# Kernel tuning notes

Measured on AMD Instinct MI355X. Metric: run time of the kernel, lower is better.

## Reference

```python
import jax, jax.numpy as jnp
import numpy as np

N = 50000      # nodes
E = 800000     # edges (avg degree 16)
C = 128        # hidden_channels
L = 3          # CGConv layers actually executed (forward uses layers[1:] of 4)
K = 10         # category_number
BN_EPS = 1e-5


def setup_inputs() -> dict:
    key = jax.random.key(0)
    ks = jax.random.split(key, 18)
    s = 0.05
    inp = {
        "x": jax.random.normal(ks[0], (N, 7), dtype=jnp.float32),
        "edge_index": jax.random.randint(ks[1], (2, E), 0, N, dtype=jnp.int64),
        "edge_attr": jax.random.normal(ks[2], (E, 6), dtype=jnp.float32),
        # node / edge encoders
        "node_W": jax.random.normal(ks[3], (C, 7), dtype=jnp.float32) * s,
        "node_b": jax.random.normal(ks[4], (C,), dtype=jnp.float32) * s,
        "edge_W": jax.random.normal(ks[5], (C, 6), dtype=jnp.float32) * s,
        "edge_b": jax.random.normal(ks[6], (C,), dtype=jnp.float32) * s,
        # CGConv layers (stacked over L): lin_f, lin_s take concat(x_i, x_j, e) of dim 3C
        "Wf": jax.random.normal(ks[7], (L, C, 3 * C), dtype=jnp.float32) * s,
        "bf": jax.random.normal(ks[8], (L, C), dtype=jnp.float32) * s,
        "Ws": jax.random.normal(ks[9], (L, C, 3 * C), dtype=jnp.float32) * s,
        "bs": jax.random.normal(ks[10], (L, C), dtype=jnp.float32) * s,
        # batch norm (eval-mode: running stats)
        "gamma": jnp.ones((L, C), dtype=jnp.float32),
        "beta": jnp.zeros((L, C), dtype=jnp.float32),
        "bn_mean": jax.random.normal(ks[11], (L, C), dtype=jnp.float32) * s,
        "bn_var": jax.random.uniform(ks[12], (L, C), dtype=jnp.float32) + 0.5,
        # classifier head
        "lin_W": jax.random.normal(ks[13], (K, C), dtype=jnp.float32) * s,
        "lin_b": jax.random.normal(ks[14], (K,), dtype=jnp.float32) * s,
    }
    return inp


def _gcn_forward(x, edge_index, edge_attr, node_W, node_b, edge_W, edge_b,
                 Wf, bf, Ws, bs, gamma, beta, bn_mean, bn_var, lin_W, lin_b):
    h = x @ node_W.T + node_b                      # [N, C]
    e = edge_attr @ edge_W.T + edge_b              # [E, C]
    src = edge_index[0]                            # x_j (source)
    dst = edge_index[1]                            # x_i (target / aggregation index)
    n = h.shape[0]
    c = h.shape[1]
    for l in range(Wf.shape[0]):
        # split concat weight: z = [x_i | x_j | e]; W z = Wi x_i + Wj x_j + We e
        Wfi, Wfj, Wfe = Wf[l, :, :c], Wf[l, :, c:2 * c], Wf[l, :, 2 * c:]
        Wsi, Wsj, Wse = Ws[l, :, :c], Ws[l, :, c:2 * c], Ws[l, :, 2 * c:]
        # node-side projections once per node, then gather per edge
        hf_i, hf_j = h @ Wfi.T, h @ Wfj.T          # [N, C]
        hs_i, hs_j = h @ Wsi.T, h @ Wsj.T
        zf = hf_i[dst] + hf_j[src] + e @ Wfe.T + bf[l]   # [E, C]
        zs = hs_i[dst] + hs_j[src] + e @ Wse.T + bs[l]
        msg = jax.nn.sigmoid(zf) * jax.nn.softplus(zs)   # CGConv gated message
        agg = jax.ops.segment_max(msg, dst, num_segments=n)  # max aggregation
        agg = jnp.where(jnp.isneginf(agg), 0.0, agg)     # nodes with no in-edges -> 0
        # batch norm (eval) on aggregated messages
        agg = (agg - bn_mean[l]) * jax.lax.rsqrt(bn_var[l] + BN_EPS) * gamma[l] + beta[l]
        h = h + agg                                       # CGConv residual
    return h @ lin_W.T + lin_b, h


def reference(x, edge_index, edge_attr, node_W, node_b, edge_W, edge_b,
              Wf, bf, Ws, bs, gamma, beta, bn_mean, bn_var, lin_W, lin_b):
    return _gcn_forward(x, edge_index, edge_attr, node_W, node_b, edge_W, edge_b,
                        Wf, bf, Ws, bs, gamma, beta, bn_mean, bn_var, lin_W, lin_b)
```

## Files before the change

### kernel.cpp

```cpp
#include <hip/hip_runtime.h>

#define N_NODES 50000
#define N_EDGES 800000
#define C 128
#define NLAYERS 3
#define KOUT 10
#define BN_EPS 1e-5f
#define NGROUP_PAD 3128
#define SBLK 196
#define MAXDEG 64
#define LOG2E 1.4426950408889634f
#define LN2   0.6931471805599453f

#if __has_builtin(__builtin_amdgcn_exp2f)
#define EXP2(x) __builtin_amdgcn_exp2f(x)
#else
#define EXP2(x) exp2f(x)
#endif
#if __has_builtin(__builtin_amdgcn_logf)
#define LOG2(x) __builtin_amdgcn_logf(x)
#else
#define LOG2(x) log2f(x)
#endif
#if __has_builtin(__builtin_amdgcn_rcpf)
#define RCP(x) __builtin_amdgcn_rcpf(x)
#else
#define RCP(x) (1.f / (x))
#endif

typedef float v2f __attribute__((ext_vector_type(2)));
typedef __attribute__((ext_vector_type(4))) float f32x4;
typedef __attribute__((ext_vector_type(8))) short s16x8;

__device__ __forceinline__ float bf2f(unsigned short u) {
    return __uint_as_float(((unsigned int)u) << 16);
}
__device__ __forceinline__ unsigned short f2bf(float f) {
    unsigned int b = __float_as_uint(f);
    b += 0x7fff + ((b >> 16) & 1);
    return (unsigned short)(b >> 16);
}
__device__ __forceinline__ float blo(unsigned int u) { return __uint_as_float(u << 16); }
__device__ __forceinline__ float bhi(unsigned int u) { return __uint_as_float(u & 0xffff0000u); }
__device__ __forceinline__ unsigned int pk2bf(float lo, float hi) {
    return (unsigned int)f2bf(lo) | ((unsigned int)f2bf(hi) << 16);
}
__device__ __forceinline__ float loadf(const void* p, long long i, int bf) {
    return bf ? bf2f(((const unsigned short*)p)[i]) : ((const float*)p)[i];
}
__device__ __forceinline__ int loadi(const void* p, long long i, int i64) {
    return i64 ? (int)((const long long*)p)[i] : ((const int*)p)[i];
}

__device__ __forceinline__ int h16f_off(int n, int chunk) {
    int g = n >> 4, rr = n & 15;
    int ks = chunk >> 2, kq = chunk & 3;
    return (((g * 4 + ks) * 64) + kq * 16 + rr) * 8;
}
__device__ __forceinline__ int perm_o(int o) {
    int g = o >> 7, c = o & 127;
    return ((g & 2) ? 256 : 0) + ((c >> 2) << 3) + ((g & 1) ? 4 : 0) + (c & 3);
}

__global__ __launch_bounds__(256) void setup_kernel(
    int* __restrict__ cnt, const unsigned int* __restrict__ gbits,
    const unsigned int* __restrict__ ebits, int* __restrict__ flags) {
    int b = blockIdx.x, t = threadIdx.x;
    if (b < SBLK) {
        int i = b * 256 + t;
        if (i < N_NODES) cnt[i] = 0;
    } else {
        __shared__ int nz;
        if (t == 0) nz = 0;
        __syncthreads();
        if (t < 63 && ebits[t * 2 + 1] != 0u) atomicAdd(&nz, 1);
        __syncthreads();
        if (t == 0) {
            flags[0] = (gbits[0] == 0x3F803F80u) ? 1 : 0;
            flags[1] = (nz == 0) ? 1 : 0;
        }
    }
}

__global__ __launch_bounds__(256) void work1_kernel(
    const void* __restrict__ x, const void* __restrict__ node_W,
    const void* __restrict__ node_b, float* __restrict__ h,
    unsigned short* __restrict__ h16f,
    const void* __restrict__ Wf, const void* __restrict__ Ws,
    const void* __restrict__ bfv, const void* __restrict__ bsv,
    const void* __restrict__ edge_W, const void* __restrict__ edge_b,
    const void* __restrict__ gamma, const void* __restrict__ beta,
    const void* __restrict__ bn_mean, const void* __restrict__ bn_var,
    const void* __restrict__ lin_W, const void* __restrict__ lin_b,
    unsigned short* __restrict__ W2, float* __restrict__ Wfold,
    float* __restrict__ bfold,
    float* __restrict__ bnA, float* __restrict__ bnB,
    float* __restrict__ linWf, float* __restrict__ linbf,
    const int* __restrict__ flags) {
    int f = flags[0];
    int b = blockIdx.x, t = threadIdx.x;
    if (b < 6250) {
        int gtid = b * 256 + t;
        int n = gtid >> 5;
        if (n >= N_NODES) return;
        int q = gtid & 31, c0 = q * 4;
        float xv[7];
#pragma unroll
        for (int j = 0; j < 7; ++j) xv[j] = loadf(x, (long long)n * 7 + j, f);
        float4 acc;
        float* ap = (float*)&acc;
#pragma unroll
        for (int i = 0; i < 4; ++i) {
            int c = c0 + i;
            float a = loadf(node_b, c, f);
#pragma unroll
            for (int j = 0; j < 7; ++j)
                a = fmaf(xv[j], loadf(node_W, (long long)c * 7 + j, f), a);
            ap[i] = a;
        }
        ((float4*)h)[(long long)n * 32 + q] = acc;
        ushort4 s;
        s.x = f2bf(ap[0]); s.y = f2bf(ap[1]); s.z = f2bf(ap[2]); s.w = f2bf(ap[3]);
        *((ushort4*)(h16f + h16f_off(n, q >> 1) + (q & 1) * 4)) = s;
    } else {
        int bb = b - 6250;
        if (bb < 768) {
            int idx = bb * 256 + t;
            int k = idx & 127;
            int o = (idx >> 7) & 511;
            int l = idx >> 16;
            int c = o & 127;
            int g = o >> 7;
            long long base = (long long)l * C * 3 * C + (long long)c * 3 * C;
            float v;
            if (g == 0)      v = loadf(Wf, base + k, f);
            else if (g == 1) v = loadf(Ws, base + k, f);
            else if (g == 2) v = loadf(Wf, base + C + k, f);
            else             v = loadf(Ws, base + C + k, f);
            v *= LOG2E;
            int p = perm_o(o);
            int rt = p >> 4, rr = p & 15;
            int ch = k >> 3, j = k & 7;
            int ks = ch >> 2, kq = ch & 3;
            size_t w2i = ((((size_t)l * 32 + rt) * 4 + ks) * 64 + kq * 16 + rr) * 8 + j;
            W2[w2i] = f2bf(v);
        } else if (bb < 774) {
            if (t >= 128) return;
            int cc = bb - 768;
            int l = cc >> 1, s = cc & 1;
            const void* W = s ? Ws : Wf;
            const void* bias = s ? bsv : bfv;
            long long wbase = (long long)l * C * 3 * C + (long long)t * 3 * C + 2 * C;
            float acc[6] = {0.f, 0.f, 0.f, 0.f, 0.f, 0.f};
            float bacc = 0.f;
            for (int k = 0; k < C; ++k) {
                float w = loadf(W, wbase + k, f);
#pragma unroll
                for (int j = 0; j < 6; ++j)
                    acc[j] = fmaf(w, loadf(edge_W, k * 6 + j, f), acc[j]);
                bacc = fmaf(w, loadf(edge_b, k, f), bacc);
            }
#pragma unroll
            for (int j = 0; j < 6; ++j) Wfold[cc * 768 + j * C + t] = acc[j] * LOG2E;
            bfold[cc * C + t] = (bacc + loadf(bias, l * C + t, f)) * LOG2E;
        } else if (bb < 779) {
            int idx = (bb - 774) * 256 + t;
            if (idx < KOUT * C) linWf[idx] = loadf(lin_W, idx, f);
            if (idx < KOUT) linbf[idx] = loadf(lin_b, idx, f);
        } else {
            int idx = (bb - 779) * 256 + t;
            if (idx < NLAYERS * C) {
                float mn = loadf(bn_mean, idx, f);
                float vr = loadf(bn_var, idx, f);
                float gm = loadf(gamma, idx, f);
                float bt = loadf(beta, idx, f);
                float a = gm * rsqrtf(vr + BN_EPS);
                bnA[idx] = a * LN2;
                bnB[idx] = bt - mn * a;
            }
        }
    }
}

__global__ __launch_bounds__(256) void scatter_kernel(
    const void* __restrict__ edge_index, const void* __restrict__ edge_attr,
    int* __restrict__ cnt, float* __restrict__ eatt,
    const int* __restrict__ flags) {
    int f = flags[0], i64 = flags[1];
    int e = blockIdx.x * blockDim.x + threadIdx.x;
    if (e >= N_EDGES) return;
    int src = loadi(edge_index, e, i64);
    int dst = loadi(edge_index, (long long)N_EDGES + e, i64);
    int pos = atomicAdd(&cnt[dst], 1);
    if (pos >= MAXDEG) return;
    uint4 E;
    if (f) {
        const unsigned short* ea = (const unsigned short*)edge_attr;
        unsigned int b0 = ea[e * 6 + 0], b1 = ea[e * 6 + 1], b2 = ea[e * 6 + 2];
        unsigned int b3 = ea[e * 6 + 3], b4 = ea[e * 6 + 4], b5 = ea[e * 6 + 5];
        E.x = b0 | (b1 << 16); E.y = b2 | (b3 << 16); E.z = b4 | (b5 << 16);
    } else {
        const float* ea = (const float*)edge_attr;
        E.x = pk2bf(ea[e * 6 + 0], ea[e * 6 + 1]);
        E.y = pk2bf(ea[e * 6 + 2], ea[e * 6 + 3]);
        E.z = pk2bf(ea[e * 6 + 4], ea[e * 6 + 5]);
    }
    E.w = (unsigned int)src;
    ((uint4*)eatt)[(size_t)dst * MAXDEG + pos] = E;
}

__global__ __launch_bounds__(256) void gemm_kernel(
    const unsigned short* __restrict__ h16f,
    const unsigned short* __restrict__ W2,
    unsigned short* __restrict__ hcat) {
    __shared__ float smem[4 * 16 * 66];
    float* ls = smem;
    int wid = threadIdx.x >> 6, lane = threadIdx.x & 63;
    int mtile = blockIdx.x >> 1;
    int n0 = (blockIdx.x & 1) * 256 + wid * 64;
    int m0 = mtile * 64, g0 = mtile * 4;
    int rt0 = n0 >> 4;
    int cw = lane & 15, kq = lane >> 4, rw = kq * 4;
    const s16x8* Ap = (const s16x8*)h16f;
    const s16x8* Bp = (const s16x8*)W2;
    f32x4 acc[4][4];
#pragma unroll
    for (int i = 0; i < 4; ++i)
#pragma unroll
        for (int j = 0; j < 4; ++j) acc[i][j] = (f32x4){0.f, 0.f, 0.f, 0.f};
#pragma unroll
    for (int ks = 0; ks < 4; ++ks) {
        s16x8 a[4], b[4];
#pragma unroll
        for (int mt = 0; mt < 4; ++mt)
            a[mt] = Ap[((g0 + mt) * 4 + ks) * 64 + lane];
#pragma unroll
        for (int nt = 0; nt < 4; ++nt)
            b[nt] = Bp[((rt0 + nt) * 4 + ks) * 64 + lane];
#pragma unroll
        for (int mt = 0; mt < 4; ++mt)
#pragma unroll
            for (int nt = 0; nt < 4; ++nt)
                acc[mt][nt] = __builtin_amdgcn_mfma_f32_16x16x32_bf16(
                    a[mt], b[nt], acc[mt][nt], 0, 0, 0);
    }
    float* lw = ls + wid * (16 * 66);
    int er = lane >> 2, ecg = lane & 3;
#pragma unroll
    for (int mt = 0; mt < 4; ++mt) {
#pragma unroll
        for (int nt = 0; nt < 4; ++nt)
#pragma unroll
            for (int reg = 0; reg < 4; ++reg)
                lw[(rw + reg) * 66 + nt * 16 + cw] = acc[mt][nt][reg];
        int m = m0 + mt * 16 + er;
        float vv[16];
#pragma unroll
        for (int t2 = 0; t2 < 8; ++t2) {
            float2 w = *((float2*)&lw[er * 66 + ecg * 16 + t2 * 2]);
            vv[t2 * 2] = w.x; vv[t2 * 2 + 1] = w.y;
        }
        if (m < N_NODES) {
            ushort4 u0, u1, u2, u3;
            u0.x=f2bf(vv[0]);  u0.y=f2bf(vv[1]);  u0.z=f2bf(vv[2]);  u0.w=f2bf(vv[3]);
            u1.x=f2bf(vv[4]);  u1.y=f2bf(vv[5]);  u1.z=f2bf(vv[6]);  u1.w=f2bf(vv[7]);
            u2.x=f2bf(vv[8]);  u2.y=f2bf(vv[9]);  u2.z=f2bf(vv[10]); u2.w=f2bf(vv[11]);
            u3.x=f2bf(vv[12]); u3.y=f2bf(vv[13]); u3.z=f2bf(vv[14]); u3.w=f2bf(vv[15]);
            ushort4* dst = (ushort4*)(hcat + (size_t)m * 512 + n0 + ecg * 16);
            dst[0] = u0; dst[1] = u1; dst[2] = u2; dst[3] = u3;
        }
    }
}

__global__ __launch_bounds__(64) void agg_kernel(
    const float* __restrict__ eatt,
    const int* __restrict__ cnt, const unsigned short* __restrict__ hcat,
    const float* __restrict__ Wfold, const float* __restrict__ bfold,
    float* __restrict__ h, unsigned short* __restrict__ h16f,
    const float* __restrict__ bnA, const float* __restrict__ bnB,
    void* __restrict__ outp,
    int layer, const int* __restrict__ flags) {
    int f = flags[0];
    int n = blockIdx.x;
    int lane = threadIdx.x & 63;
    int half = lane >> 5;
    int q = lane & 31;
    int c0 = q * 4;

    float4 bA = *((const float4*)(bnA + layer * C + c0));
    float4 bB = *((const float4*)(bnB + layer * C + c0));
    int d = cnt[n];
    if (d > MAXDEG) d = MAXDEG;
    float mf[4] = {0.f, 0.f, 0.f, 0.f};

    const float* wfp = Wfold + (2 * layer + 0) * 768;
    const float* wsp = Wfold + (2 * layer + 1) * 768;
    v2f wf2[6][2], ws2[6][2];
#pragma unroll
    for (int j = 0; j < 6; ++j) {
        float4 a = *((const float4*)(wfp + j * C + c0));
        float4 b = *((const float4*)(wsp + j * C + c0));
        wf2[j][0] = (v2f){a.x, a.y}; wf2[j][1] = (v2f){a.z, a.w};
        ws2[j][0] = (v2f){b.x, b.y}; ws2[j][1] = (v2f){b.z, b.w};
    }
    float4 bfv = *((const float4*)(bfold + (2 * layer + 0) * C + c0));
    float4 bsv = *((const float4*)(bfold + (2 * layer + 1) * C + c0));
    uint4 ib = ((const uint4*)hcat)[(long long)n * 64 + q];
    v2f bf0 = (v2f){blo(ib.x) + bfv.x, bhi(ib.x) + bfv.y};
    v2f bf1 = (v2f){blo(ib.y) + bfv.z, bhi(ib.y) + bfv.w};
    v2f bs0 = (v2f){blo(ib.z) + bsv.x, bhi(ib.z) + bsv.y};
    v2f bs1 = (v2f){blo(ib.w) + bsv.z, bhi(ib.w) + bsv.w};

    auto body = [&](v2f hf0, v2f hf1, v2f hs0, v2f hs1, const float* ea) {
        v2f vf0 = bf0 + hf0, vf1 = bf1 + hf1;
        v2f vs0 = bs0 + hs0, vs1 = bs1 + hs1;
#pragma unroll
        for (int j = 0; j < 6; ++j) {
            v2f ej = (v2f){ea[j], ea[j]};
            vf0 = __builtin_elementwise_fma(ej, wf2[j][0], vf0);
            vf1 = __builtin_elementwise_fma(ej, wf2[j][1], vf1);
            vs0 = __builtin_elementwise_fma(ej, ws2[j][0], vs0);
            vs1 = __builtin_elementwise_fma(ej, ws2[j][1], vs1);
        }
        float zf[4] = {vf0.x, vf0.y, vf1.x, vf1.y};
        float zs[4] = {vs0.x, vs0.y, vs1.x, vs1.y};
#pragma unroll
        for (int i = 0; i < 4; ++i) {
            float sg = RCP(1.f + EXP2(-zf[i]));
            float sp = fmaxf(zs[i], 0.f) + LOG2(1.f + EXP2(-fabsf(zs[i])));
            mf[i] = fmaxf(mf[i], sg * sp);
        }
    };

    const uint4* hb = (const uint4*)hcat;
    const uint4* ep = (const uint4*)eatt + (size_t)n * MAXDEG;
    for (int p = half; p < d; p += 2) {
        uint4 E = ep[p];
        uint4 jb = hb[(long long)E.w * 64 + 32 + q];
        float ea[6] = {blo(E.x), bhi(E.x), blo(E.y), bhi(E.y), blo(E.z), bhi(E.z)};
        body((v2f){blo(jb.x), bhi(jb.x)}, (v2f){blo(jb.y), bhi(jb.y)},
             (v2f){blo(jb.z), bhi(jb.z)}, (v2f){blo(jb.w), bhi(jb.w)}, ea);
    }
#pragma unroll
    for (int i = 0; i < 4; ++i) mf[i] = fmaxf(mf[i], __shfl_xor(mf[i], 32));

    if (half == 0) {
        float4 hv = ((float4*)h)[(long long)n * 32 + q];
        float* hp = (float*)&hv;
        const float* bAp = (const float*)&bA;
        const float* bBp = (const float*)&bB;
#pragma unroll
        for (int i = 0; i < 4; ++i)
            hp[i] += mf[i] * bAp[i] + bBp[i];
        ((float4*)h)[(long long)n * 32 + q] = hv;
        {
            ushort4 s;
            s.x = f2bf(hp[0]); s.y = f2bf(hp[1]); s.z = f2bf(hp[2]); s.w = f2bf(hp[3]);
            *((ushort4*)(h16f + h16f_off(n, q >> 1) + (q & 1) * 4)) = s;
        }
        if (layer == NLAYERS - 1) {
            if (f) {
                ushort4 s;
                s.x = f2bf(hp[0]); s.y = f2bf(hp[1]); s.z = f2bf(hp[2]); s.w = f2bf(hp[3]);
                *((ushort4*)((unsigned short*)outp + N_NODES * KOUT + n * C + c0)) = s;
            } else {
                *((float4*)((float*)outp + N_NODES * KOUT + n * C + c0)) = hv;
            }
        }
    }
}

__global__ __launch_bounds__(256) void out_kernel(
    const float* __restrict__ h, const float* __restrict__ linWf,
    const float* __restrict__ linbf, void* __restrict__ out,
    const int* __restrict__ flags) {
    int f = flags[0];
    int g = blockIdx.x * 16 + (threadIdx.x >> 4);
    int l16 = threadIdx.x & 15;
    if (g >= N_NODES) return;
    const float4* hr = (const float4*)(h + (long long)g * C) + l16 * 2;
    float4 a0 = hr[0], a1 = hr[1];
    float res = 0.f;
#pragma unroll
    for (int k = 0; k < KOUT; ++k) {
        const float4* wr = (const float4*)(linWf + (long long)k * C) + l16 * 2;
        float4 w0 = wr[0], w1 = wr[1];
        float p = a0.x * w0.x + a0.y * w0.y + a0.z * w0.z + a0.w * w0.w
                + a1.x * w1.x + a1.y * w1.y + a1.z * w1.z + a1.w * w1.w;
        p += __shfl_xor(p, 1); p += __shfl_xor(p, 2);
        p += __shfl_xor(p, 4); p += __shfl_xor(p, 8);
        if (l16 == k) res = p + linbf[k];
    }
    if (l16 < KOUT) {
        long long idx = (long long)g * KOUT + l16;
        if (f) ((unsigned short*)out)[idx] = f2bf(res);
        else   ((float*)out)[idx] = res;
    }
}

extern "C" void kernel_launch(void* const* d_in, const int* in_sizes, int n_in,
                              void* d_out, int out_size, void* d_ws, size_t ws_size,
                              hipStream_t stream) {
    const void* x          = d_in[0];
    const void* edge_index = d_in[1];
    const void* edge_attr  = d_in[2];
    const void* node_W     = d_in[3];
    const void* node_b     = d_in[4];
    const void* edge_W     = d_in[5];
    const void* edge_b     = d_in[6];
    const void* Wf         = d_in[7];
    const void* bf         = d_in[8];
    const void* Ws         = d_in[9];
    const void* bs         = d_in[10];
    const void* gamma      = d_in[11];
    const void* beta       = d_in[12];
    const void* bn_mean    = d_in[13];
    const void* bn_var     = d_in[14];
    const void* lin_W      = d_in[15];
    const void* lin_b      = d_in[16];

    const size_t sz_h    = (size_t)N_NODES * C * 4;
    const size_t sz_h16f = (size_t)NGROUP_PAD * 4 * 64 * 8 * 2;
    const size_t sz_hc16 = (size_t)N_NODES * 512 * 2;
    const size_t sz_w2   = (size_t)NLAYERS * 512 * C * 2;
    const size_t sz_eatt = (size_t)N_NODES * MAXDEG * 16;

    char* wsp = (char*)d_ws;
    size_t off = 0;
    auto alloc = [&](size_t bytes) -> void* {
        void* p = wsp + off; off += (bytes + 255) & ~(size_t)255; return p;
    };
    float*          h      = (float*)alloc(sz_h);
    unsigned short* h16f   = (unsigned short*)alloc(sz_h16f);
    unsigned short* hcat   = (unsigned short*)alloc(sz_hc16);
    int*            cnt    = (int*)alloc((size_t)N_NODES * 4);
    float*          eatt   = (float*)alloc(sz_eatt);
    unsigned short* W2     = (unsigned short*)alloc(sz_w2);
    float*          Wfold  = (float*)alloc(6 * 768 * 4);
    float*          bfold  = (float*)alloc(6 * C * 4);
    float*          bnA    = (float*)alloc(NLAYERS * C * 4);
    float*          bnB    = (float*)alloc(NLAYERS * C * 4);
    float*          linWf  = (float*)alloc(KOUT * C * 4);
    float*          linbf  = (float*)alloc(KOUT * 4);
    int*            flags  = (int*)alloc(256);

    setup_kernel<<<SBLK + 1, 256, 0, stream>>>(
        cnt, (const unsigned int*)gamma, (const unsigned int*)edge_index, flags);
    scatter_kernel<<<3125, 256, 0, stream>>>(
        edge_index, edge_attr, cnt, eatt, flags);
    work1_kernel<<<7031, 256, 0, stream>>>(
        x, node_W, node_b, h, h16f,
        Wf, Ws, bf, bs, edge_W, edge_b, gamma, beta, bn_mean, bn_var,
        lin_W, lin_b, W2, Wfold, bfold, bnA, bnB, linWf, linbf, flags);

    for (int l = 0; l < NLAYERS; ++l) {
        gemm_kernel<<<1564, 256, 0, stream>>>(
            h16f, W2 + (size_t)l * 512 * C, hcat);
        agg_kernel<<<N_NODES, 64, 0, stream>>>(
            eatt, cnt, hcat, Wfold, bfold, h, h16f,
            bnA, bnB, d_out, l, flags);
    }
    out_kernel<<<(N_NODES + 15) / 16, 256, 0, stream>>>(
        h, linWf, linbf, d_out, flags);
}
```

Measured before the change: 673.1 us.

## Fuse edge scatter into first-layer GEMM launch and pack two nodes per agg block

The separate edge scatter kernel is removed. Its blocks are interleaved with the first layer's GEMM blocks in one launch, two scatter blocks for every GEMM block, so the atomic bucketing of edges can overlap with the MFMA projection and one launch is saved. The aggregation kernel now runs two nodes per 128-thread block instead of one node per 64-thread block, which halves the block count. The interleaving mixes memory-bound and compute-bound blocks in one grid, which can change occupancy. The agg change assumes N_NODES is even for full coverage, which holds here.

```diff
diff --git a/kernel.cpp b/kernel.cpp
--- a/kernel.cpp
+++ b/kernel.cpp
@@ -182,42 +182,51 @@
     }
 }
 
-__global__ __launch_bounds__(256) void scatter_kernel(
-    const void* __restrict__ edge_index, const void* __restrict__ edge_attr,
-    int* __restrict__ cnt, float* __restrict__ eatt,
-    const int* __restrict__ flags) {
-    int f = flags[0], i64 = flags[1];
-    int e = blockIdx.x * blockDim.x + threadIdx.x;
-    if (e >= N_EDGES) return;
-    int src = loadi(edge_index, e, i64);
-    int dst = loadi(edge_index, (long long)N_EDGES + e, i64);
-    int pos = atomicAdd(&cnt[dst], 1);
-    if (pos >= MAXDEG) return;
-    uint4 E;
-    if (f) {
-        const unsigned short* ea = (const unsigned short*)edge_attr;
-        unsigned int b0 = ea[e * 6 + 0], b1 = ea[e * 6 + 1], b2 = ea[e * 6 + 2];
-        unsigned int b3 = ea[e * 6 + 3], b4 = ea[e * 6 + 4], b5 = ea[e * 6 + 5];
-        E.x = b0 | (b1 << 16); E.y = b2 | (b3 << 16); E.z = b4 | (b5 << 16);
-    } else {
-        const float* ea = (const float*)edge_attr;
-        E.x = pk2bf(ea[e * 6 + 0], ea[e * 6 + 1]);
-        E.y = pk2bf(ea[e * 6 + 2], ea[e * 6 + 3]);
-        E.z = pk2bf(ea[e * 6 + 4], ea[e * 6 + 5]);
-    }
-    E.w = (unsigned int)src;
-    ((uint4*)eatt)[(size_t)dst * MAXDEG + pos] = E;
-}
-
 __global__ __launch_bounds__(256) void gemm_kernel(
     const unsigned short* __restrict__ h16f,
     const unsigned short* __restrict__ W2,
-    unsigned short* __restrict__ hcat) {
+    unsigned short* __restrict__ hcat,
+    const void* __restrict__ edge_index, const void* __restrict__ edge_attr,
+    int* __restrict__ cnt, float* __restrict__ eatt,
+    const int* __restrict__ flags, int do_scatter) {
     __shared__ float smem[4 * 16 * 66];
+    int b = blockIdx.x;
+    int gid;
+    if (do_scatter) {
+        int m3 = b % 3;
+        if (m3 != 0) {
+            int sid = (b / 3) * 2 + m3 - 1;
+            if (sid >= 3125) return;
+            int f = flags[0], i64 = flags[1];
+            int e = sid * 256 + threadIdx.x;
+            int src = loadi(edge_index, e, i64);
+            int dst = loadi(edge_index, (long long)N_EDGES + e, i64);
+            int pos = atomicAdd(&cnt[dst], 1);
+            if (pos >= MAXDEG) return;
+            uint4 E;
+            if (f) {
+                const unsigned short* ea = (const unsigned short*)edge_attr;
+                unsigned int b0 = ea[e * 6 + 0], b1 = ea[e * 6 + 1], b2 = ea[e * 6 + 2];
+                unsigned int b3 = ea[e * 6 + 3], b4 = ea[e * 6 + 4], b5 = ea[e * 6 + 5];
+                E.x = b0 | (b1 << 16); E.y = b2 | (b3 << 16); E.z = b4 | (b5 << 16);
+            } else {
+                const float* ea = (const float*)edge_attr;
+                E.x = pk2bf(ea[e * 6 + 0], ea[e * 6 + 1]);
+                E.y = pk2bf(ea[e * 6 + 2], ea[e * 6 + 3]);
+                E.z = pk2bf(ea[e * 6 + 4], ea[e * 6 + 5]);
+            }
+            E.w = (unsigned int)src;
+            ((uint4*)eatt)[(size_t)dst * MAXDEG + pos] = E;
+            return;
+        }
+        gid = b / 3;
+    } else {
+        gid = b;
+    }
     float* ls = smem;
     int wid = threadIdx.x >> 6, lane = threadIdx.x & 63;
-    int mtile = blockIdx.x >> 1;
-    int n0 = (blockIdx.x & 1) * 256 + wid * 64;
+    int mtile = gid >> 1;
+    int n0 = (gid & 1) * 256 + wid * 64;
     int m0 = mtile * 64, g0 = mtile * 4;
     int rt0 = n0 >> 4;
     int cw = lane & 15, kq = lane >> 4, rw = kq * 4;
@@ -230,19 +239,19 @@
         for (int j = 0; j < 4; ++j) acc[i][j] = (f32x4){0.f, 0.f, 0.f, 0.f};
 #pragma unroll
     for (int ks = 0; ks < 4; ++ks) {
-        s16x8 a[4], b[4];
+        s16x8 a[4], bfr[4];
 #pragma unroll
         for (int mt = 0; mt < 4; ++mt)
             a[mt] = Ap[((g0 + mt) * 4 + ks) * 64 + lane];
 #pragma unroll
         for (int nt = 0; nt < 4; ++nt)
-            b[nt] = Bp[((rt0 + nt) * 4 + ks) * 64 + lane];
+            bfr[nt] = Bp[((rt0 + nt) * 4 + ks) * 64 + lane];
 #pragma unroll
         for (int mt = 0; mt < 4; ++mt)
 #pragma unroll
             for (int nt = 0; nt < 4; ++nt)
                 acc[mt][nt] = __builtin_amdgcn_mfma_f32_16x16x32_bf16(
-                    a[mt], b[nt], acc[mt][nt], 0, 0, 0);
+                    a[mt], bfr[nt], acc[mt][nt], 0, 0, 0);
     }
     float* lw = ls + wid * (16 * 66);
     int er = lane >> 2, ecg = lane & 3;
@@ -272,7 +281,7 @@
     }
 }
 
-__global__ __launch_bounds__(64) void agg_kernel(
+__global__ __launch_bounds__(128) void agg_kernel(
     const float* __restrict__ eatt,
     const int* __restrict__ cnt, const unsigned short* __restrict__ hcat,
     const float* __restrict__ Wfold, const float* __restrict__ bfold,
@@ -281,7 +290,8 @@
     void* __restrict__ outp,
     int layer, const int* __restrict__ flags) {
     int f = flags[0];
-    int n = blockIdx.x;
+    int n = blockIdx.x * 2 + (threadIdx.x >> 6);
+    if (n >= N_NODES) return;
     int lane = threadIdx.x & 63;
     int half = lane >> 5;
     int q = lane & 31;
@@ -446,17 +456,17 @@
 
     setup_kernel<<<SBLK + 1, 256, 0, stream>>>(
         cnt, (const unsigned int*)gamma, (const unsigned int*)edge_index, flags);
-    scatter_kernel<<<3125, 256, 0, stream>>>(
-        edge_index, edge_attr, cnt, eatt, flags);
     work1_kernel<<<7031, 256, 0, stream>>>(
         x, node_W, node_b, h, h16f,
         Wf, Ws, bf, bs, edge_W, edge_b, gamma, beta, bn_mean, bn_var,
         lin_W, lin_b, W2, Wfold, bfold, bnA, bnB, linWf, linbf, flags);
 
     for (int l = 0; l < NLAYERS; ++l) {
-        gemm_kernel<<<1564, 256, 0, stream>>>(
-            h16f, W2 + (size_t)l * 512 * C, hcat);
-        agg_kernel<<<N_NODES, 64, 0, stream>>>(
+        int do_sc = (l == 0) ? 1 : 0;
+        gemm_kernel<<<do_sc ? 4692 : 1564, 256, 0, stream>>>(
+            h16f, W2 + (size_t)l * 512 * C, hcat,
+            edge_index, edge_attr, cnt, eatt, flags, do_sc);
+        agg_kernel<<<N_NODES / 2, 128, 0, stream>>>(
             eatt, cnt, hcat, Wfold, bfold, h, h16f,
             bnA, bnB, d_out, l, flags);
     }
```

Measured after the change: 680.7 us. Within noise of the previous version (+1.1%).
